# Kernel tuning notes

Measured on AMD Instinct MI355X. Metric: run time of the kernel, lower is better.

The kernel has to match this reference:

```python
import jax, jax.numpy as jnp
import numpy as np

B, S, D, H, HID = 4, 2048, 1024, 16, 4096
DK = D // H
EPS = 1e-6


def layernorm(x, alpha, bias):
    # Matches the custom LayerNorm: std with Bessel correction (torch default),
    # and eps added to std (not variance).
    mean = jnp.mean(x, axis=-1, keepdims=True)
    std = jnp.std(x, axis=-1, ddof=1, keepdims=True)
    return alpha * (x - mean) / (std + EPS) + bias


def setup_inputs() -> dict:
    key = jax.random.key(0)
    ks = jax.random.split(key, 10)
    s = 0.02
    return {
        "x": jax.random.normal(ks[0], (B, S, D), dtype=jnp.float32),
        "wq": jax.random.normal(ks[1], (D, D), dtype=jnp.float32) * s,
        "wk": jax.random.normal(ks[2], (D, D), dtype=jnp.float32) * s,
        "wv": jax.random.normal(ks[3], (D, D), dtype=jnp.float32) * s,
        "wo": jax.random.normal(ks[4], (D, D), dtype=jnp.float32) * s,
        "w1": jax.random.normal(ks[5], (D, HID), dtype=jnp.float32) * s,
        "b1": jnp.zeros((HID,), dtype=jnp.float32),
        "w2": jax.random.normal(ks[6], (HID, D), dtype=jnp.float32) * s,
        "b2": jnp.zeros((D,), dtype=jnp.float32),
        "ln1_a": jnp.ones((D,), dtype=jnp.float32),
        "ln1_b": jnp.zeros((D,), dtype=jnp.float32),
        "ln2_a": jnp.ones((D,), dtype=jnp.float32),
        "ln2_b": jnp.zeros((D,), dtype=jnp.float32),
    }


def reference(x, wq, wk, wv, wo, w1, b1, w2, b2, ln1_a, ln1_b, ln2_a, ln2_b):
    # --- residual 1: pre-norm self-attention ---
    h = layernorm(x, ln1_a, ln1_b)
    q = (h @ wq).reshape(B, S, H, DK)
    k = (h @ wk).reshape(B, S, H, DK)
    v = (h @ wv).reshape(B, S, H, DK)
    scores = jnp.einsum("bqhd,bkhd->bhqk", q, k) / jnp.sqrt(jnp.float32(DK))
    # Faithful replication of the original mask: tril on a (1, max_len) matrix
    # keeps only key position 0; all other key positions get -1e9.
    key_keep = (jnp.arange(S) == 0)  # [S]
    scores = jnp.where(key_keep[None, None, None, :], scores, jnp.float32(-1e9))
    attn = jax.nn.softmax(scores, axis=-1)  # [B,H,S,S]
    ctx = jnp.einsum("bhqk,bkhd->bqhd", attn, v).reshape(B, S, D)
    x = x + ctx @ wo
    # --- residual 2: pre-norm FFN ---
    h2 = layernorm(x, ln2_a, ln2_b)
    ff = jax.nn.gelu(h2 @ w1 + b1, approximate=False) @ w2 + b2
    return x + ff
```

## Files before the change

kernel.cpp:

```cpp
#include <hip/hip_runtime.h>
#include <cstdint>

#define D_MODEL 1024
#define HIDDEN  4096
#define BATCH   4
#define SEQ     2048
#define NROWS   (BATCH*SEQ)

typedef __attribute__((ext_vector_type(4))) int i32x4;

#define ACT_AMAX 4.0f
#define ACT_S    (ACT_AMAX / 127.0f)
#define ACT_INV  (127.0f / ACT_AMAX)

#define GLDS16(g, l) __builtin_amdgcn_global_load_lds(                        \
    (const __attribute__((address_space(1))) unsigned int*)(g),               \
    (__attribute__((address_space(3))) unsigned int*)(l), 16, 0, 0)

__device__ __forceinline__ float block_sum(float v, float* s4) {
  #pragma unroll
  for (int off = 32; off > 0; off >>= 1) v += __shfl_down(v, off);
  int lane = threadIdx.x & 63, wid = threadIdx.x >> 6;
  __syncthreads();
  if (lane == 0) s4[wid] = v;
  __syncthreads();
  return s4[0] + s4[1] + s4[2] + s4[3];
}

__device__ __forceinline__ float block_max(float v, float* s4) {
  #pragma unroll
  for (int off = 32; off > 0; off >>= 1) v = fmaxf(v, __shfl_down(v, off));
  int lane = threadIdx.x & 63, wid = threadIdx.x >> 6;
  __syncthreads();
  if (lane == 0) s4[wid] = v;
  __syncthreads();
  return fmaxf(fmaxf(s4[0], s4[1]), fmaxf(s4[2], s4[3]));
}

__device__ __forceinline__ signed char qclamp(float v) {
  float r = rintf(v);
  r = fminf(127.f, fmaxf(-127.f, r));
  return (signed char)(int)r;
}

#define KCHUNKS 32
#define KCH     (D_MODEL / KCHUNKS)


__device__ __forceinline__ void absmax_cols_body(
    const float* __restrict__ in, int R, int C, unsigned* __restrict__ u,
    int bx, int by) {
  int c  = bx * 256 + threadIdx.x;
  int r0 = by * 64;
  float m = 0.f;
  #pragma unroll 4
  for (int r = 0; r < 64; ++r)
    m = fmaxf(m, fabsf(in[(size_t)(r0 + r) * C + c]));
  atomicMax(&u[c], __float_as_uint(m));
}

__device__ __forceinline__ void transpose_quant_body(
    const float* __restrict__ in, signed char* __restrict__ out,
    int R, int C, const unsigned* __restrict__ u,
    float (*tile)[33], int bx, int by) {
  int c0 = bx * 32, r0 = by * 32;
  int tx = threadIdx.x & 31, ty = threadIdx.x >> 5;
  #pragma unroll
  for (int i = ty; i < 32; i += 8)
    tile[i][tx] = in[(size_t)(r0 + i) * C + c0 + tx];
  __syncthreads();
  #pragma unroll
  for (int i = ty; i < 32; i += 8) {
    float f = __uint_as_float(u[c0 + i]);
    float inv = f > 0.f ? 127.f / f : 0.f;
    out[(size_t)(c0 + i) * R + r0 + tx] = qclamp(tile[tx][i] * inv);
  }
}

__device__ __forceinline__ void ln_matvec_body(
    const float* __restrict__ x, const float* __restrict__ ln_a,
    const float* __restrict__ ln_b, const float* __restrict__ W,
    float* __restrict__ vout, float* s4, float (*hs)[KCH], int bx, int by) {
  int n  = bx * 256 + threadIdx.x;
  int k0 = by * KCH;
  int t  = threadIdx.x;
  float4 g4 = ((const float4*)ln_a)[t];
  float4 b4 = ((const float4*)ln_b)[t];
  #pragma unroll
  for (int b = 0; b < 4; ++b) {
    const float* xr = x + (size_t)b * SEQ * D_MODEL;
    float4 v = ((const float4*)xr)[t];
    float sum = v.x + v.y + v.z + v.w;
    float mean = block_sum(sum, s4) * (1.f / 1024.f);
    float cx = v.x - mean, cy = v.y - mean, cz = v.z - mean, cw = v.w - mean;
    float sq = cx * cx + cy * cy + cz * cz + cw * cw;
    float var = block_sum(sq, s4) * (1.f / 1023.f);
    float inv = 1.f / (sqrtf(var) + 1e-6f);
    if (t >= (k0 >> 2) && t < ((k0 + KCH) >> 2)) {
      int lc = 4 * t - k0;
      hs[b][lc + 0] = g4.x * cx * inv + b4.x;
      hs[b][lc + 1] = g4.y * cy * inv + b4.y;
      hs[b][lc + 2] = g4.z * cz * inv + b4.z;
      hs[b][lc + 3] = g4.w * cw * inv + b4.w;
    }
  }
  __syncthreads();
  float a0 = 0, a1 = 0, a2 = 0, a3 = 0;
  #pragma unroll
  for (int k = 0; k < KCH; ++k) {
    float w = W[(size_t)(k0 + k) * D_MODEL + n];
    a0 = fmaf(hs[0][k], w, a0);
    a1 = fmaf(hs[1][k], w, a1);
    a2 = fmaf(hs[2][k], w, a2);
    a3 = fmaf(hs[3][k], w, a3);
  }
  atomicAdd(&vout[0 * D_MODEL + n], a0);
  atomicAdd(&vout[1 * D_MODEL + n], a1);
  atomicAdd(&vout[2 * D_MODEL + n], a2);
  atomicAdd(&vout[3 * D_MODEL + n], a3);
}

__device__ __forceinline__ void matvec_body(
    const float* __restrict__ vin, const float* __restrict__ W,
    float* __restrict__ vout, float (*hs)[KCH], int bx, int by) {
  int n  = bx * 256 + threadIdx.x;
  int k0 = by * KCH;
  if (threadIdx.x < 4 * KCH)
    hs[threadIdx.x / KCH][threadIdx.x % KCH] =
        vin[(threadIdx.x / KCH) * D_MODEL + k0 + (threadIdx.x % KCH)];
  __syncthreads();
  float a0 = 0, a1 = 0, a2 = 0, a3 = 0;
  #pragma unroll
  for (int k = 0; k < KCH; ++k) {
    float w = W[(size_t)(k0 + k) * D_MODEL + n];
    a0 = fmaf(hs[0][k], w, a0);
    a1 = fmaf(hs[1][k], w, a1);
    a2 = fmaf(hs[2][k], w, a2);
    a3 = fmaf(hs[3][k], w, a3);
  }
  atomicAdd(&vout[0 * D_MODEL + n], a0);
  atomicAdd(&vout[1 * D_MODEL + n], a1);
  atomicAdd(&vout[2 * D_MODEL + n], a2);
  atomicAdd(&vout[3 * D_MODEL + n], a3);
}

__global__ __launch_bounds__(256) void pre1(
    const float* __restrict__ w1, const float* __restrict__ w2,
    unsigned* __restrict__ u1, unsigned* __restrict__ u2,
    const float* __restrict__ x, const float* __restrict__ ln1a,
    const float* __restrict__ ln1b, const float* __restrict__ wv,
    float* __restrict__ v0) {
  __shared__ float s4[4];
  __shared__ float hs[4][KCH];
  int id = blockIdx.x;
  if (id < 256) {
    absmax_cols_body(w1, D_MODEL, HIDDEN, u1, id & 15, id >> 4);
  } else if (id < 512) {
    int r = id - 256;
    absmax_cols_body(w2, HIDDEN, D_MODEL, u2, r & 3, r >> 2);
  } else {
    int r = id - 512;
    ln_matvec_body(x, ln1a, ln1b, wv, v0, s4, hs, r & 3, r >> 2);
  }
}

__global__ __launch_bounds__(256) void pre2(
    const float* __restrict__ w1, const float* __restrict__ w2,
    const unsigned* __restrict__ u1, const unsigned* __restrict__ u2,
    signed char* __restrict__ w1t, signed char* __restrict__ w2t,
    const float* __restrict__ v0, const float* __restrict__ wo,
    float* __restrict__ delta) {
  __shared__ float tile[32][33];
  __shared__ float hs[4][KCH];
  int id = blockIdx.x;
  if (id < 4096) {
    transpose_quant_body(w1, w1t, D_MODEL, HIDDEN, u1, tile, id & 127, id >> 7);
  } else if (id < 8192) {
    int r = id - 4096;
    transpose_quant_body(w2, w2t, HIDDEN, D_MODEL, u2, tile, r & 31, r >> 5);
  } else {
    int r = id - 8192;
    matvec_body(v0, wo, delta, hs, r & 3, r >> 2);
  }
}

__global__ __launch_bounds__(256) void fused_res_ln_q(
    const float* __restrict__ x, const float* __restrict__ delta,
    const float* __restrict__ g, const float* __restrict__ be,
    float* __restrict__ x1_out, signed char* __restrict__ h2,
    float* __restrict__ hscale) {
  __shared__ float s4[4];
  int row = blockIdx.x;
  int b = row >> 11;
  int t = threadIdx.x;
  float4 v  = ((const float4*)(x + (size_t)row * D_MODEL))[t];
  float4 d4 = ((const float4*)(delta + (size_t)b * D_MODEL))[t];
  v.x += d4.x; v.y += d4.y; v.z += d4.z; v.w += d4.w;
  float sum = v.x + v.y + v.z + v.w;
  float mean = block_sum(sum, s4) * (1.f / 1024.f);
  float cx = v.x - mean, cy = v.y - mean, cz = v.z - mean, cw = v.w - mean;
  float sq = cx * cx + cy * cy + cz * cz + cw * cw;
  float var = block_sum(sq, s4) * (1.f / 1023.f);
  float inv = 1.f / (sqrtf(var) + 1e-6f);
  ((float4*)(x1_out + (size_t)row * D_MODEL))[t] = v;
  float4 g4 = ((const float4*)g)[t];
  float4 b4 = ((const float4*)be)[t];
  float h0v = g4.x * cx * inv + b4.x;
  float h1v = g4.y * cy * inv + b4.y;
  float h2v = g4.z * cz * inv + b4.z;
  float h3v = g4.w * cw * inv + b4.w;
  float am = fmaxf(fmaxf(fabsf(h0v), fabsf(h1v)), fmaxf(fabsf(h2v), fabsf(h3v)));
  float amax = block_max(am, s4);
  float qs = amax > 0.f ? 127.f / amax : 0.f;
  unsigned q = ((unsigned)(unsigned char)(int)qclamp(h0v * qs)) |
               ((unsigned)(unsigned char)(int)qclamp(h1v * qs) << 8) |
               ((unsigned)(unsigned char)(int)qclamp(h2v * qs) << 16) |
               ((unsigned)(unsigned char)(int)qclamp(h3v * qs) << 24);
  ((unsigned*)(h2 + (size_t)row * D_MODEL))[t] = q;
  if (t == 0) hscale[row] = amax * (1.f / 127.f);
}

__global__ __launch_bounds__(256, 2) void gemm1_t4(
    const signed char* __restrict__ A, const signed char* __restrict__ Bt,
    const float* __restrict__ rowS, const unsigned* __restrict__ colU,
    const float* __restrict__ bias, signed char* __restrict__ Cq,
    int M, int N, int K) {
  __shared__ signed char LA[2][128][128];
  __shared__ signed char LB[2][128][128];

  int GN  = N / 128;
  int CX  = (GN >= 16) ? 16 : (GN >> 1);
  int id  = blockIdx.x;
  int xcd = id & 7;
  int r   = id >> 3;
  int cby = xcd >> 1, cbx = xcd & 1;
  int lby = r / CX,   lbx = r % CX;
  int by  = cby * 16 + lby;
  int bx  = cbx * CX + lbx;
  int m0  = by * 128, n0 = bx * 128;
  int NT  = K / 128;

  int t = threadIdx.x;
  int wid = t >> 6, lane = t & 63;
  int wm = wid >> 1, wn = wid & 1;
  int lr = lane & 15, kg = lane >> 4;
  int swz = (lr & 7) << 4;

  int rS = t >> 3;
  int cS = ((t & 7) ^ (rS & 7)) * 16;
  const signed char* Ag = A  + (size_t)(m0 + rS) * K + cS;
  const signed char* Bg = Bt + (size_t)(n0 + rS) * K + cS;
  int ldsOff = wid * 1024;

#define G1_STG(s, T) do {                                                      \
    size_t ko_ = (size_t)(T) * 128;                                            \
    GLDS16(Ag + ko_,                  &LA[s][0][0] + ldsOff);                  \
    GLDS16(Ag + ko_ + (size_t)32 * K, &LA[s][0][0] + ldsOff + 4096);           \
    GLDS16(Ag + ko_ + (size_t)64 * K, &LA[s][0][0] + ldsOff + 8192);           \
    GLDS16(Ag + ko_ + (size_t)96 * K, &LA[s][0][0] + ldsOff + 12288);          \
    GLDS16(Bg + ko_,                  &LB[s][0][0] + ldsOff);                  \
    GLDS16(Bg + ko_ + (size_t)32 * K, &LB[s][0][0] + ldsOff + 4096);           \
    GLDS16(Bg + ko_ + (size_t)64 * K, &LB[s][0][0] + ldsOff + 8192);           \
    GLDS16(Bg + ko_ + (size_t)96 * K, &LB[s][0][0] + ldsOff + 12288);          \
  } while (0)

#define G1_RD(s) do {                                                          \
    _Pragma("unroll") for (int mi = 0; mi < 4; ++mi)                           \
    _Pragma("unroll") for (int kk = 0; kk < 2; ++kk)                           \
      a[mi][kk] = *(const i32x4*)                                              \
          &LA[s][wm * 64 + mi * 16 + lr][(kk * 64 + kg * 16) ^ swz];           \
    _Pragma("unroll") for (int ni = 0; ni < 4; ++ni)                           \
    _Pragma("unroll") for (int kk = 0; kk < 2; ++kk)                           \
      b[ni][kk] = *(const i32x4*)                                              \
          &LB[s][wn * 64 + ni * 16 + lr][(kk * 64 + kg * 16) ^ swz];           \
  } while (0)

#define G1_MM() do {                                                           \
    _Pragma("unroll") for (int mi = 0; mi < 4; ++mi)                           \
    _Pragma("unroll") for (int ni = 0; ni < 4; ++ni)                           \
    _Pragma("unroll") for (int kk = 0; kk < 2; ++kk)                           \
      acc[mi][ni] = __builtin_amdgcn_mfma_i32_16x16x64_i8(                     \
          a[mi][kk], b[ni][kk], acc[mi][ni], 0, 0, 0);                         \
  } while (0)

  i32x4 acc[4][4] = {};
  i32x4 a[4][2];
  i32x4 b[4][2];

  G1_STG(0, 0);
  for (int tt = 0; tt < NT; ++tt) {
    int s = tt & 1;
    int tn = tt + 1 < NT ? tt + 1 : NT - 1;
    G1_STG(s ^ 1, tn);
    asm volatile("s_waitcnt vmcnt(8)" ::: "memory");
    __builtin_amdgcn_s_barrier();
    G1_RD(s);
    G1_MM();
    __builtin_amdgcn_s_barrier();
  }
  asm volatile("s_waitcnt vmcnt(0)" ::: "memory");

  int orow = m0 + wm * 64;
  int ocol = n0 + wn * 64;
  #pragma unroll
  for (int mf = 0; mf < 4; ++mf) {
    #pragma unroll
    for (int nf = 0; nf < 4; ++nf) {
      int col = ocol + nf * 16 + lr;
      float cs = __uint_as_float(colU[col]) * (1.f / 127.f);
      float bz = bias[col];
      #pragma unroll
      for (int j = 0; j < 4; ++j) {
        int row = orow + mf * 16 + kg * 4 + j;
        float rs = rowS[row];
        float val = (float)acc[mf][nf][j] * rs * cs + bz;
        float u = val * (0.7978845608f + 0.0356774081f * val * val);
        float e = __expf(2.f * u);
        float th = 1.f - 2.f / (e + 1.f);
        val = 0.5f * val * (1.f + th);
        Cq[(size_t)row * N + col] = qclamp(val * ACT_INV);
      }
    }
  }
#undef G1_STG
#undef G1_RD
#undef G1_MM
}

__global__ __launch_bounds__(256, 2) void gemm2_t4(
    const signed char* __restrict__ A, const signed char* __restrict__ Bt,
    const unsigned* __restrict__ colU, const float* __restrict__ bias,
    float* __restrict__ Cf, int M, int N, int K) {
  __shared__ signed char LA[2][128][128];
  __shared__ signed char LB[2][128][128];

  int GN  = N / 128;
  int CX  = (GN >= 16) ? 16 : (GN >> 1);
  int id  = blockIdx.x;
  int xcd = id & 7;
  int r   = id >> 3;
  int cby = xcd >> 1, cbx = xcd & 1;
  int lby = r / CX,   lbx = r % CX;
  int by  = cby * 16 + lby;
  int bx  = cbx * CX + lbx;
  int m0  = by * 128, n0 = bx * 128;
  int NT  = K / 128;

  int t = threadIdx.x;
  int wid = t >> 6, lane = t & 63;
  int wm = wid >> 1, wn = wid & 1;
  int lr = lane & 15, kg = lane >> 4;
  int swz = (lr & 7) << 4;

  int rS = t >> 3;
  int cS = ((t & 7) ^ (rS & 7)) * 16;
  const signed char* Ag = A  + (size_t)(m0 + rS) * K + cS;
  const signed char* Bg = Bt + (size_t)(n0 + rS) * K + cS;
  int ldsOff = wid * 1024;

#define G2_STG(s, T) do {                                                      \
    size_t ko_ = (size_t)(T) * 128;                                            \
    GLDS16(Ag + ko_,                  &LA[s][0][0] + ldsOff);                  \
    GLDS16(Ag + ko_ + (size_t)32 * K, &LA[s][0][0] + ldsOff + 4096);           \
    GLDS16(Ag + ko_ + (size_t)64 * K, &LA[s][0][0] + ldsOff + 8192);           \
    GLDS16(Ag + ko_ + (size_t)96 * K, &LA[s][0][0] + ldsOff + 12288);          \
    GLDS16(Bg + ko_,                  &LB[s][0][0] + ldsOff);                  \
    GLDS16(Bg + ko_ + (size_t)32 * K, &LB[s][0][0] + ldsOff + 4096);           \
    GLDS16(Bg + ko_ + (size_t)64 * K, &LB[s][0][0] + ldsOff + 8192);           \
    GLDS16(Bg + ko_ + (size_t)96 * K, &LB[s][0][0] + ldsOff + 12288);          \
  } while (0)

#define G2_RD(s) do {                                                          \
    _Pragma("unroll") for (int mi = 0; mi < 4; ++mi)                           \
    _Pragma("unroll") for (int kk = 0; kk < 2; ++kk)                           \
      a[mi][kk] = *(const i32x4*)                                              \
          &LA[s][wm * 64 + mi * 16 + lr][(kk * 64 + kg * 16) ^ swz];           \
    _Pragma("unroll") for (int ni = 0; ni < 4; ++ni)                           \
    _Pragma("unroll") for (int kk = 0; kk < 2; ++kk)                           \
      b[ni][kk] = *(const i32x4*)                                              \
          &LB[s][wn * 64 + ni * 16 + lr][(kk * 64 + kg * 16) ^ swz];           \
  } while (0)

#define G2_MM() do {                                                           \
    _Pragma("unroll") for (int mi = 0; mi < 4; ++mi)                           \
    _Pragma("unroll") for (int ni = 0; ni < 4; ++ni)                           \
    _Pragma("unroll") for (int kk = 0; kk < 2; ++kk)                           \
      acc[mi][ni] = __builtin_amdgcn_mfma_i32_16x16x64_i8(                     \
          a[mi][kk], b[ni][kk], acc[mi][ni], 0, 0, 0);                         \
  } while (0)

  i32x4 acc[4][4] = {};
  i32x4 a[4][2];
  i32x4 b[4][2];

  G2_STG(0, 0);
  for (int tt = 0; tt < NT; ++tt) {
    int s = tt & 1;
    int tn = tt + 1 < NT ? tt + 1 : NT - 1;
    G2_STG(s ^ 1, tn);
    asm volatile("s_waitcnt vmcnt(8)" ::: "memory");
    __builtin_amdgcn_s_barrier();
    G2_RD(s);
    G2_MM();
    __builtin_amdgcn_s_barrier();
  }
  asm volatile("s_waitcnt vmcnt(0)" ::: "memory");

  int orow = m0 + wm * 64;
  int ocol = n0 + wn * 64;
  #pragma unroll
  for (int mf = 0; mf < 4; ++mf) {
    #pragma unroll
    for (int nf = 0; nf < 4; ++nf) {
      int col = ocol + nf * 16 + lr;
      float cs = __uint_as_float(colU[col]) * (1.f / 127.f);
      float bz = bias[col];
      #pragma unroll
      for (int j = 0; j < 4; ++j) {
        int row = orow + mf * 16 + kg * 4 + j;
        float val = (float)acc[mf][nf][j] * ACT_S * cs + bz;
        size_t idx = (size_t)row * N + col;
        Cf[idx] = Cf[idx] + val;
      }
    }
  }
#undef G2_STG
#undef G2_RD
#undef G2_MM
}

extern "C" void kernel_launch(void* const* d_in, const int* in_sizes, int n_in,
                              void* d_out, int out_size, void* d_ws, size_t ws_size,
                              hipStream_t stream) {
  const float* x    = (const float*)d_in[0];
  const float* wv   = (const float*)d_in[3];
  const float* wo   = (const float*)d_in[4];
  const float* w1   = (const float*)d_in[5];
  const float* b1   = (const float*)d_in[6];
  const float* w2   = (const float*)d_in[7];
  const float* b2   = (const float*)d_in[8];
  const float* ln1a = (const float*)d_in[9];
  const float* ln1b = (const float*)d_in[10];
  const float* ln2a = (const float*)d_in[11];
  const float* ln2b = (const float*)d_in[12];
  float* out = (float*)d_out;

  char* ws = (char*)d_ws;
  signed char* w1t = (signed char*)(ws);
  signed char* w2t = (signed char*)(ws + (4ull  << 20));
  signed char* h2  = (signed char*)(ws + (8ull  << 20));
  signed char* act = (signed char*)(ws + (16ull << 20));
  char* sc = ws + (48ull << 20);
  unsigned* u1    = (unsigned*)(sc);
  unsigned* u2    = (unsigned*)(sc + 16384);
  float*    v0    = (float*)(sc + 20480);
  float*    delta = (float*)(sc + 36864);
  float*    hsc   = (float*)(sc + 53248);

  hipMemsetAsync(sc, 0, 53248, stream);

  pre1<<<640, 256, 0, stream>>>(w1, w2, u1, u2, x, ln1a, ln1b, wv, v0);

  pre2<<<8320, 256, 0, stream>>>(w1, w2, u1, u2, w1t, w2t, v0, wo, delta);

  fused_res_ln_q<<<NROWS, 256, 0, stream>>>(x, delta, ln2a, ln2b, out, h2, hsc);

  gemm1_t4<<<(NROWS / 128) * (HIDDEN / 128), 256, 0, stream>>>(
      h2, w1t, hsc, u1, b1, act, NROWS, HIDDEN, D_MODEL);

  gemm2_t4<<<(NROWS / 128) * (D_MODEL / 128), 256, 0, stream>>>(
      act, w2t, u2, b2, out, NROWS, D_MODEL, HIDDEN);
}
```

Baseline: 164.8 us.

## Drop LDS double buffering in gemm1 to raise occupancy to three blocks

Replaces the double-buffered LDS staging in the first FFN int8 GEMM with a single buffer. Each iteration now loads a tile, waits for all loads, computes, then barriers. This halves LDS use per block to 32 KB and raises the launch-bounds occupancy hint from 2 to 3, relying on more resident blocks to hide memory latency instead of the software prefetch. The cost is that loads and MFMA work inside a block no longer overlap.

```diff
diff --git a/kernel.cpp b/kernel.cpp
--- a/kernel.cpp
+++ b/kernel.cpp
@@ -220,13 +220,13 @@
   if (t == 0) hscale[row] = amax * (1.f / 127.f);
 }
 
-__global__ __launch_bounds__(256, 2) void gemm1_t4(
+__global__ __launch_bounds__(256, 3) void gemm1_k128(
     const signed char* __restrict__ A, const signed char* __restrict__ Bt,
     const float* __restrict__ rowS, const unsigned* __restrict__ colU,
     const float* __restrict__ bias, signed char* __restrict__ Cq,
     int M, int N, int K) {
-  __shared__ signed char LA[2][128][128];
-  __shared__ signed char LB[2][128][128];
+  __shared__ signed char LA[128][128];
+  __shared__ signed char LB[128][128];
 
   int GN  = N / 128;
   int CX  = (GN >= 16) ? 16 : (GN >> 1);
@@ -252,27 +252,27 @@
   const signed char* Bg = Bt + (size_t)(n0 + rS) * K + cS;
   int ldsOff = wid * 1024;
 
-#define G1_STG(s, T) do {                                                      \
+#define G1_STG(T) do {                                                         \
     size_t ko_ = (size_t)(T) * 128;                                            \
-    GLDS16(Ag + ko_,                  &LA[s][0][0] + ldsOff);                  \
-    GLDS16(Ag + ko_ + (size_t)32 * K, &LA[s][0][0] + ldsOff + 4096);           \
-    GLDS16(Ag + ko_ + (size_t)64 * K, &LA[s][0][0] + ldsOff + 8192);           \
-    GLDS16(Ag + ko_ + (size_t)96 * K, &LA[s][0][0] + ldsOff + 12288);          \
-    GLDS16(Bg + ko_,                  &LB[s][0][0] + ldsOff);                  \
-    GLDS16(Bg + ko_ + (size_t)32 * K, &LB[s][0][0] + ldsOff + 4096);           \
-    GLDS16(Bg + ko_ + (size_t)64 * K, &LB[s][0][0] + ldsOff + 8192);           \
-    GLDS16(Bg + ko_ + (size_t)96 * K, &LB[s][0][0] + ldsOff + 12288);          \
-  } while (0)
-
-#define G1_RD(s) do {                                                          \
+    GLDS16(Ag + ko_,                  &LA[0][0] + ldsOff);                     \
+    GLDS16(Ag + ko_ + (size_t)32 * K, &LA[0][0] + ldsOff + 4096);              \
+    GLDS16(Ag + ko_ + (size_t)64 * K, &LA[0][0] + ldsOff + 8192);              \
+    GLDS16(Ag + ko_ + (size_t)96 * K, &LA[0][0] + ldsOff + 12288);             \
+    GLDS16(Bg + ko_,                  &LB[0][0] + ldsOff);                     \
+    GLDS16(Bg + ko_ + (size_t)32 * K, &LB[0][0] + ldsOff + 4096);              \
+    GLDS16(Bg + ko_ + (size_t)64 * K, &LB[0][0] + ldsOff + 8192);              \
+    GLDS16(Bg + ko_ + (size_t)96 * K, &LB[0][0] + ldsOff + 12288);             \
+  } while (0)
+
+#define G1_RD() do {                                                           \
     _Pragma("unroll") for (int mi = 0; mi < 4; ++mi)                           \
     _Pragma("unroll") for (int kk = 0; kk < 2; ++kk)                           \
       a[mi][kk] = *(const i32x4*)                                              \
-          &LA[s][wm * 64 + mi * 16 + lr][(kk * 64 + kg * 16) ^ swz];           \
+          &LA[wm * 64 + mi * 16 + lr][(kk * 64 + kg * 16) ^ swz];              \
     _Pragma("unroll") for (int ni = 0; ni < 4; ++ni)                           \
     _Pragma("unroll") for (int kk = 0; kk < 2; ++kk)                           \
       b[ni][kk] = *(const i32x4*)                                              \
-          &LB[s][wn * 64 + ni * 16 + lr][(kk * 64 + kg * 16) ^ swz];           \
+          &LB[wn * 64 + ni * 16 + lr][(kk * 64 + kg * 16) ^ swz];              \
   } while (0)
 
 #define G1_MM() do {                                                           \
@@ -287,18 +287,14 @@
   i32x4 a[4][2];
   i32x4 b[4][2];
 
-  G1_STG(0, 0);
   for (int tt = 0; tt < NT; ++tt) {
-    int s = tt & 1;
-    int tn = tt + 1 < NT ? tt + 1 : NT - 1;
-    G1_STG(s ^ 1, tn);
-    asm volatile("s_waitcnt vmcnt(8)" ::: "memory");
+    G1_STG(tt);
+    asm volatile("s_waitcnt vmcnt(0)" ::: "memory");
     __builtin_amdgcn_s_barrier();
-    G1_RD(s);
+    G1_RD();
     G1_MM();
     __builtin_amdgcn_s_barrier();
   }
-  asm volatile("s_waitcnt vmcnt(0)" ::: "memory");
 
   int orow = m0 + wm * 64;
   int ocol = n0 + wn * 64;
@@ -465,7 +461,7 @@
 
   fused_res_ln_q<<<NROWS, 256, 0, stream>>>(x, delta, ln2a, ln2b, out, h2, hsc);
 
-  gemm1_t4<<<(NROWS / 128) * (HIDDEN / 128), 256, 0, stream>>>(
+  gemm1_k128<<<(NROWS / 128) * (HIDDEN / 128), 256, 0, stream>>>(
       h2, w1t, hsc, u1, b1, act, NROWS, HIDDEN, D_MODEL);
 
   gemm2_t4<<<(NROWS / 128) * (D_MODEL / 128), 256, 0, stream>>>(
```

Result: slower. 168.9 us (+2.5%).
